# Kernel optimization log

Hardware: AMD Instinct MI355X
Metric: run time of the kernel (lower is better)

## Reference

```python
import jax, jax.numpy as jnp
import numpy as np

D_MODEL, D_K, D_V, N_HEADS = 1024, 64, 64, 16
B, S = 2, 2048
LN_EPS = 1e-5


def setup_inputs() -> dict:
    key = jax.random.key(0)
    ks = jax.random.split(key, 12)
    s = 1.0 / np.sqrt(D_MODEL)
    inp = {
        "Q": jax.random.normal(ks[0], (B, S, D_MODEL), jnp.float32),
        "K": jax.random.normal(ks[1], (B, S, D_MODEL), jnp.float32),
        "V": jax.random.normal(ks[2], (B, S, D_MODEL), jnp.float32),
        "attn_mask": jax.random.bernoulli(ks[3], 0.1, (B, S, S)),
        "Wq": jax.random.uniform(ks[4], (D_MODEL, D_K * N_HEADS), jnp.float32, -s, s),
        "bq": jnp.zeros((D_K * N_HEADS,), jnp.float32),
        "Wk": jax.random.uniform(ks[5], (D_MODEL, D_K * N_HEADS), jnp.float32, -s, s),
        "bk": jnp.zeros((D_K * N_HEADS,), jnp.float32),
        "Wv": jax.random.uniform(ks[6], (D_MODEL, D_V * N_HEADS), jnp.float32, -s, s),
        "bv": jnp.zeros((D_V * N_HEADS,), jnp.float32),
        "Wo": jax.random.uniform(ks[7], (N_HEADS * D_V, D_MODEL), jnp.float32, -s, s),
        "bo": jnp.zeros((D_MODEL,), jnp.float32),
        "gamma": jnp.ones((D_MODEL,), jnp.float32),
        "beta": jnp.zeros((D_MODEL,), jnp.float32),
    }
    return inp


def reference(Q, K, V, attn_mask, Wq, bq, Wk, bk, Wv, bv, Wo, bo, gamma, beta):
    b, s, _ = Q.shape
    # projections -> [B, S, H, d]
    q = (Q @ Wq + bq).reshape(b, s, N_HEADS, D_K)
    k = (K @ Wk + bk).reshape(b, -1, N_HEADS, D_K)
    v = (V @ Wv + bv).reshape(b, -1, N_HEADS, D_V)
    # scores [B, H, Sq, Sk]
    scores = jnp.einsum("bqhd,bkhd->bhqk", q, k) / np.sqrt(D_K).astype(np.float32)
    scores = jnp.where(attn_mask[:, None, :, :], jnp.float32(-1e9), scores)
    attn = jax.nn.softmax(scores, axis=-1)
    context = jnp.einsum("bhqk,bkhd->bqhd", attn, v).reshape(b, s, N_HEADS * D_V)
    out = context @ Wo + bo + Q  # residual
    mu = jnp.mean(out, axis=-1, keepdims=True)
    var = jnp.var(out, axis=-1, keepdims=True)
    return (out - mu) * jax.lax.rsqrt(var + LN_EPS) * gamma + beta
```

## Files before the change

kernel.cpp:

```cpp
#include <hip/hip_runtime.h>
#include <hip/hip_bf16.h>
#include <math.h>


#define D_MODEL 1024
#define NHEADS  16
#define DHEAD   64
#define BATCH   2
#define SEQ     2048
#define MROWS   (BATCH * SEQ)
#define SCLF    0.18033688f

typedef __attribute__((ext_vector_type(8)))  short bf16x8;
typedef __attribute__((ext_vector_type(4)))  float f32x4;
typedef __attribute__((ext_vector_type(16))) float f32x16;

__device__ inline unsigned short f2bf(float f) {
    unsigned int u = __builtin_bit_cast(unsigned int, f);
    unsigned int r = (u + 0x7FFFu + ((u >> 16) & 1u)) >> 16;
    return (unsigned short)r;
}

__device__ inline unsigned cvtpk_bf16(float lo, float hi2) {
    unsigned r;
    asm("v_cvt_pk_bf16_f32 %0, %1, %2" : "=v"(r) : "v"(lo), "v"(hi2));
    return r;
}

__device__ inline void gload16(const unsigned short* g, unsigned short* lbase, int lane) {
#if __has_builtin(__builtin_amdgcn_global_load_lds)
    __builtin_amdgcn_global_load_lds(
        (const __attribute__((address_space(1))) unsigned int*)g,
        (__attribute__((address_space(3))) unsigned int*)lbase, 16, 0, 0);
#else
    *(bf16x8*)(lbase + lane * 8) = *(const bf16x8*)g;
#endif
}

__global__ __launch_bounds__(256) void detect_mask_par(
    const unsigned int* __restrict__ m, int nwords, int* __restrict__ flags)
{
    const int i = blockIdx.x * 256 + threadIdx.x;
    int a = 0, b = 0;
    if (i < nwords) {
        const unsigned int w = m[i];
        a = (w != 0u && w != 1u);
        b = (w != 0u && w != 0x3F800000u);
    }
    const int wa = (int)__any(a);
    const int wb = (int)__any(b);
    if ((threadIdx.x & 63) == 0) {
        if (wa) atomicOr(&flags[0], 1);
        if (wb) atomicOr(&flags[1], 1);
    }
}

__global__ __launch_bounds__(256) void pack_mask_ballot(
    const void* __restrict__ mask, const int* __restrict__ flags,
    unsigned long long* __restrict__ mbits, int nwords)
{
    const int lane   = threadIdx.x & 63;
    const int wv     = blockIdx.x * 4 + (threadIdx.x >> 6);
    const int nwaves = gridDim.x * 4;
    const int mf = (flags[0] == 0) ? 0 : (flags[1] == 0) ? 1 : 2;
    for (int w = wv; w < nwords; w += nwaves) {
        bool bit;
        if (mf == 0)      bit = ((const unsigned int*)mask)[(size_t)w * 64 + lane] != 0u;
        else if (mf == 1) bit = ((const float*)mask)[(size_t)w * 64 + lane] != 0.f;
        else              bit = ((const unsigned char*)mask)[(size_t)w * 64 + lane] != 0;
        const unsigned long long b = __ballot(bit);
        if (lane == 0) mbits[w] = b;
    }
}

__global__ __launch_bounds__(256) void cvt_all(
    const float* __restrict__ Q, const float* __restrict__ K,
    const float* __restrict__ V,
    const float* __restrict__ w0, const float* __restrict__ w1,
    const float* __restrict__ w2, const float* __restrict__ w3,
    unsigned short* __restrict__ Qb, unsigned short* __restrict__ Kb,
    unsigned short* __restrict__ Vb,
    unsigned short* __restrict__ t0, unsigned short* __restrict__ t1,
    unsigned short* __restrict__ t2, unsigned short* __restrict__ t3)
{
    __shared__ float tile[64][65];
    const int z = blockIdx.z;
    if (z < 3) {
        const float* s = (z == 0) ? Q : (z == 1) ? K : V;
        unsigned short* d = (z == 0) ? Qb : (z == 1) ? Kb : Vb;
        const int i = blockIdx.x * 256 + threadIdx.x;
        float4 a = ((const float4*)s)[i * 2];
        float4 b = ((const float4*)s)[i * 2 + 1];
        unsigned u0 = cvtpk_bf16(a.x, a.y);
        unsigned u1 = cvtpk_bf16(a.z, a.w);
        unsigned u2 = cvtpk_bf16(b.x, b.y);
        unsigned u3 = cvtpk_bf16(b.z, b.w);
        ((int4*)d)[i] = make_int4((int)u0, (int)u1, (int)u2, (int)u3);
    } else {
        if (blockIdx.x >= 256) return;
        const int wz = z - 3;
        const float* W = (wz == 0) ? w0 : (wz == 1) ? w1 : (wz == 2) ? w2 : w3;
        unsigned short* T = (wz == 0) ? t0 : (wz == 1) ? t1 : (wz == 2) ? t2 : t3;
        const int n0 = (blockIdx.x & 15) * 64;
        const int k0 = (blockIdx.x >> 4) * 64;
        const int t  = threadIdx.x;
        const int r  = t >> 4;
        const int c4 = (t & 15) * 4;
        #pragma unroll
        for (int u = 0; u < 4; ++u) {
            float4 v = *(const float4*)(W + (size_t)(k0 + r + u * 16) * D_MODEL + n0 + c4);
            tile[r + u * 16][c4 + 0] = v.x;
            tile[r + u * 16][c4 + 1] = v.y;
            tile[r + u * 16][c4 + 2] = v.z;
            tile[r + u * 16][c4 + 3] = v.w;
        }
        __syncthreads();
        #pragma unroll
        for (int u = 0; u < 4; ++u) {
            const int nr = r + u * 16;
            ushort4 o;
            o.x = f2bf(tile[c4 + 0][nr]);
            o.y = f2bf(tile[c4 + 1][nr]);
            o.z = f2bf(tile[c4 + 2][nr]);
            o.w = f2bf(tile[c4 + 3][nr]);
            *(ushort4*)(T + (size_t)(n0 + nr) * D_MODEL + k0 + c4) = o;
        }
    }
}

#define BKQ 32
__global__ __launch_bounds__(256, 1) void gemm_qkv(
    const unsigned short* __restrict__ A0, const unsigned short* __restrict__ A1,
    const unsigned short* __restrict__ A2,
    const unsigned short* __restrict__ B0, const unsigned short* __restrict__ B1,
    const unsigned short* __restrict__ B2,
    const float* __restrict__ bias0, const float* __restrict__ bias1,
    const float* __restrict__ bias2,
    unsigned short* __restrict__ C0, unsigned short* __restrict__ C1,
    unsigned short* __restrict__ C2)
{
    const int z = blockIdx.z;
    const unsigned short* A  = (z == 0) ? A0 : (z == 1) ? A1 : A2;
    const unsigned short* Bt = (z == 0) ? B0 : (z == 1) ? B1 : B2;
    const float* bias        = (z == 0) ? bias0 : (z == 1) ? bias1 : bias2;
    unsigned short* C        = (z == 0) ? C0 : (z == 1) ? C1 : C2;
    const int K = D_MODEL, N = D_MODEL;

    __shared__ unsigned short As[2][128 * BKQ];
    __shared__ unsigned short Bs[2][128 * BKQ];
    const int tid  = threadIdx.x;
    const int w    = tid >> 6;
    const int lane = tid & 63;
    const int lo   = lane & 15;
    const int hi   = lane >> 4;
    const int wm   = (w >> 1) * 64;
    const int wn   = (w & 1) * 64;
    const int m0   = blockIdx.x * 128;
    const int n0   = blockIdx.y * 128;

    const unsigned short* Ab = A  + (size_t)m0 * K;
    const unsigned short* Bb = Bt + (size_t)n0 * K;

    f32x4 acc[4][4];
    #pragma unroll
    for (int i = 0; i < 4; ++i)
        #pragma unroll
        for (int j = 0; j < 4; ++j) acc[i][j] = (f32x4){0.f, 0.f, 0.f, 0.f};

    const int NT = K / BKQ;
    auto stage = [&](int buf, int t) {
        const int k0 = t * BKQ;
        #pragma unroll
        for (int i = 0; i < 2; ++i) {
            const int c = i * 256 + tid;
            gload16(Ab + (size_t)(c >> 2) * K + k0 + (c & 3) * 8,
                    &As[buf][(i * 256 + w * 64) * 8], lane);
        }
        #pragma unroll
        for (int i = 0; i < 2; ++i) {
            const int c = i * 256 + tid;
            gload16(Bb + (size_t)(c >> 2) * K + k0 + (c & 3) * 8,
                    &Bs[buf][(i * 256 + w * 64) * 8], lane);
        }
    };

    stage(0, 0);
    __syncthreads();
    int cur = 0;
    for (int t = 0; t < NT; ++t) {
        if (t + 1 < NT) stage(cur ^ 1, t + 1);
        bf16x8 af[4], bfr[4];
        #pragma unroll
        for (int f = 0; f < 4; ++f) {
            af[f]  = *(const bf16x8*)&As[cur][(wm + f * 16 + lo) * BKQ + hi * 8];
            bfr[f] = *(const bf16x8*)&Bs[cur][(wn + f * 16 + lo) * BKQ + hi * 8];
        }
        #pragma unroll
        for (int fm = 0; fm < 4; ++fm)
            #pragma unroll
            for (int fn = 0; fn < 4; ++fn)
                acc[fm][fn] = __builtin_amdgcn_mfma_f32_16x16x32_bf16(
                    af[fm], bfr[fn], acc[fm][fn], 0, 0, 0);
        __syncthreads();
        cur ^= 1;
    }

    #pragma unroll
    for (int fm = 0; fm < 4; ++fm) {
        const int row = m0 + wm + fm * 16 + hi * 4;
        #pragma unroll
        for (int fn = 0; fn < 4; ++fn) {
            const int col = n0 + wn + fn * 16 + lo;
            const float bv = bias[col];
            #pragma unroll
            for (int r = 0; r < 4; ++r) {
                float o = acc[fm][fn][r] + bv;
                if (z == 0) o *= SCLF;
                if (z < 2)
                    C[(size_t)(row + r) * N + col] = f2bf(o);
                else
                    C[(size_t)((row + r) >> 11) * 2097152
                      + (size_t)col * 2048 + ((row + r) & 2047)] = f2bf(o);
            }
        }
    }
}

__global__ __launch_bounds__(256) void gemm_out32(
    const unsigned short* __restrict__ A, const unsigned short* __restrict__ Bt,
    const float* __restrict__ bias, const float* __restrict__ resid,
    float* __restrict__ C)
{
    const int K = D_MODEL, N = D_MODEL;
    __shared__ unsigned short As[2][64 * 32];
    __shared__ unsigned short Bs[2][64 * 32];
    const int tid  = threadIdx.x;
    const int w    = tid >> 6;
    const int lane = tid & 63;
    const int lo   = lane & 15;
    const int hi   = lane >> 4;
    const int wm   = (w >> 1) * 32;
    const int wn   = (w & 1) * 32;
    const int m0   = blockIdx.x * 64;
    const int n0   = blockIdx.y * 64;

    const unsigned short* Ab = A  + (size_t)m0 * K;
    const unsigned short* Bb = Bt + (size_t)n0 * K;

    f32x4 acc[2][2];
    #pragma unroll
    for (int i = 0; i < 2; ++i)
        #pragma unroll
        for (int j = 0; j < 2; ++j) acc[i][j] = (f32x4){0.f, 0.f, 0.f, 0.f};

    const int NT = K / 32;
    auto stage = [&](int buf, int t) {
        const int k0 = t * 32;
        gload16(Ab + (size_t)(tid >> 2) * K + k0 + (tid & 3) * 8,
                &As[buf][(w * 64) * 8], lane);
        gload16(Bb + (size_t)(tid >> 2) * K + k0 + (tid & 3) * 8,
                &Bs[buf][(w * 64) * 8], lane);
    };

    stage(0, 0);
    __syncthreads();
    int cur = 0;
    for (int t = 0; t < NT; ++t) {
        if (t + 1 < NT) stage(cur ^ 1, t + 1);
        bf16x8 af[2], bfr[2];
        #pragma unroll
        for (int f = 0; f < 2; ++f) {
            af[f]  = *(const bf16x8*)&As[cur][(wm + f * 16 + lo) * 32 + hi * 8];
            bfr[f] = *(const bf16x8*)&Bs[cur][(wn + f * 16 + lo) * 32 + hi * 8];
        }
        #pragma unroll
        for (int fm = 0; fm < 2; ++fm)
            #pragma unroll
            for (int fn = 0; fn < 2; ++fn)
                acc[fm][fn] = __builtin_amdgcn_mfma_f32_16x16x32_bf16(
                    af[fm], bfr[fn], acc[fm][fn], 0, 0, 0);
        __syncthreads();
        cur ^= 1;
    }

    #pragma unroll
    for (int fm = 0; fm < 2; ++fm) {
        const int row = m0 + wm + fm * 16 + hi * 4;
        #pragma unroll
        for (int fn = 0; fn < 2; ++fn) {
            const int col = n0 + wn + fn * 16 + lo;
            const float bv = bias[col];
            #pragma unroll
            for (int r = 0; r < 4; ++r)
                C[(size_t)(row + r) * N + col] =
                    acc[fm][fn][r] + bv + resid[(size_t)(row + r) * N + col];
        }
    }
}

__global__ __launch_bounds__(512, 2) void attn_mfma32(
    const unsigned short* __restrict__ qb, const unsigned short* __restrict__ kbm,
    const unsigned short* __restrict__ vt,
    const unsigned long long* __restrict__ mbits, unsigned short* __restrict__ ctx)
{
    __shared__ __align__(16) unsigned char smem[34304];
    const int tid  = threadIdx.x;
    const int w8   = tid >> 6;
    const int g    = w8 >> 2;
    const int wq   = w8 & 3;
    const int lane = tid & 63;
    const int l31  = lane & 31;
    const int hi   = lane >> 5;
    const int h    = blockIdx.x;
    const int q0   = blockIdx.y * 128;
    const int b    = blockIdx.z;

    unsigned short* KsG = (unsigned short*)smem + (size_t)g * 4096;
    unsigned short* VsG = (unsigned short*)(smem + 16384) + (size_t)g * 4096;

    const size_t qkbase = (size_t)b * SEQ * D_MODEL + (size_t)h * DHEAD;
    const size_t vtbase = ((size_t)b * D_MODEL + h * DHEAD) * SEQ;

    const int qtok = q0 + wq * 32 + l31;
    bf16x8 qA[4];
    #pragma unroll
    for (int s = 0; s < 4; ++s)
        qA[s] = *(const bf16x8*)(qb + qkbase + (size_t)qtok * D_MODEL + s * 16 + hi * 8);

    const int4 ones_i = make_int4(0x3F803F80, 0x3F803F80, 0x3F803F80, 0x3F803F80);
    const bf16x8 ones = __builtin_bit_cast(bf16x8, ones_i);

    f32x16 o0 = {}, o1 = {}, accl = {};

    const unsigned long long* mrow = mbits + ((size_t)b * SEQ + qtok) * (SEQ / 64);

    const int krow = wq * 8 + (lane >> 3);
    const int kc   = lane & 7;
    const int kswz = kc ^ (krow & 7);
    const int vrow = wq * 16 + (lane >> 2);
    const int vsrc = ((lane & 3) - (vrow >> 1)) & 3;

    const unsigned short* kl = kbm + qkbase + (size_t)(g * 1024 + krow) * D_MODEL + kswz * 8;
    const unsigned short* vl = vt + vtbase + (size_t)vrow * SEQ + g * 1024 + vsrc * 8;
    const int kldb = (wq * 8) * 64;
    const int vldb = (wq * 16) * 32;

    auto stage = [&](int buf) {
        gload16(kl, &KsG[buf * 2048 + kldb], lane);
        gload16(vl, &VsG[buf * 2048 + vldb], lane);
        kl += (size_t)32 * D_MODEL;
        vl += 32;
    };

    stage(0);
    unsigned long long mw64 = mrow[g * 16];
    __syncthreads();
    int cur = 0;

    for (int t = 0; t < 32; ++t) {
        if (t + 1 < 32) stage(cur ^ 1);
        const unsigned int mw = (unsigned int)(mw64 >> (32 * (t & 1) + 4 * hi));
        if ((t & 1) && t + 1 < 32) mw64 = mrow[g * 16 + ((t + 1) >> 1)];

        f32x16 st = {};
        __builtin_amdgcn_s_setprio(1);
        #pragma unroll
        for (int s = 0; s < 4; ++s) {
            bf16x8 kf = *(const bf16x8*)&KsG[cur * 2048 + l31 * 64 + ((2 * s + hi) ^ (l31 & 7)) * 8];
            st = __builtin_amdgcn_mfma_f32_32x32x16_bf16(kf, qA[s], st, 0, 0, 0);
        }
        __builtin_amdgcn_s_setprio(0);

        #pragma unroll
        for (int r = 0; r < 16; ++r) {
            const int klo = (r & 3) + 8 * (r >> 2);
            const float x = ((mw >> klo) & 1u) ? -1e9f : st[r];
            st[r] = exp2f(x);
        }

        bf16x8 pa[2];
        #pragma unroll
        for (int s = 0; s < 2; ++s) {
            const int base = s * 8;
            unsigned av  = cvtpk_bf16(st[base + 0], st[base + 1]);
            unsigned bv2 = cvtpk_bf16(st[base + 4], st[base + 5]);
            unsigned cv  = cvtpk_bf16(st[base + 2], st[base + 3]);
            unsigned dv  = cvtpk_bf16(st[base + 6], st[base + 7]);
            asm("v_permlane32_swap_b32 %0, %1" : "+v"(av), "+v"(bv2));
            asm("v_permlane32_swap_b32 %0, %1" : "+v"(cv), "+v"(dv));
            int4 pk = make_int4((int)av, (int)cv, (int)bv2, (int)dv);
            pa[s] = __builtin_bit_cast(bf16x8, pk);
        }

        __builtin_amdgcn_s_setprio(1);
        #pragma unroll
        for (int s = 0; s < 2; ++s) {
            const int slot = ((2 * s + hi) + (l31 >> 1)) & 3;
            bf16x8 vf0 = *(const bf16x8*)&VsG[cur * 2048 + l31 * 32 + slot * 8];
            o0 = __builtin_amdgcn_mfma_f32_32x32x16_bf16(pa[s], vf0, o0, 0, 0, 0);
            bf16x8 vf1 = *(const bf16x8*)&VsG[cur * 2048 + (32 + l31) * 32 + slot * 8];
            o1 = __builtin_amdgcn_mfma_f32_32x32x16_bf16(pa[s], vf1, o1, 0, 0, 0);
            accl = __builtin_amdgcn_mfma_f32_32x32x16_bf16(pa[s], ones, accl, 0, 0, 0);
        }
        __builtin_amdgcn_s_setprio(0);
        __syncthreads();
        cur ^= 1;
    }

    __syncthreads();
    float* comb  = (float*)smem;
    float* lvals = (float*)(smem + 33792);
    if (g == 1) {
        float* p = comb + (size_t)(wq * 64 + lane) * 33;
        #pragma unroll
        for (int r = 0; r < 16; ++r) { p[r] = o0[r]; p[16 + r] = o1[r]; }
        if (l31 == 0) {
            #pragma unroll
            for (int r = 0; r < 16; ++r)
                lvals[wq * 32 + (r & 3) + 8 * (r >> 2) + 4 * hi] = accl[r];
        }
    }
    __syncthreads();
    if (g == 0) {
        const float* p = comb + (size_t)(wq * 64 + lane) * 33;
        #pragma unroll
        for (int r = 0; r < 16; ++r) {
            const int qloc = (r & 3) + 8 * (r >> 2) + 4 * hi;
            const float inv = 1.f / (accl[r] + lvals[wq * 32 + qloc]);
            unsigned short* dst = ctx + qkbase + (size_t)(q0 + wq * 32 + qloc) * D_MODEL;
            dst[l31]      = f2bf((o0[r] + p[r]) * inv);
            dst[32 + l31] = f2bf((o1[r] + p[16 + r]) * inv);
        }
    }
}

__global__ __launch_bounds__(256) void layernorm1024(
    const float* __restrict__ x, const float* __restrict__ gamma,
    const float* __restrict__ beta, float* __restrict__ out)
{
    const int row = blockIdx.x;
    const int tid = threadIdx.x;
    const float* xr = x + (size_t)row * D_MODEL;
    float4 v = *(const float4*)(xr + (tid << 2));
    float s = v.x + v.y + v.z + v.w;
    float q = v.x * v.x + v.y * v.y + v.z * v.z + v.w * v.w;
    #pragma unroll
    for (int off = 1; off < 64; off <<= 1) {
        s += __shfl_xor(s, off, 64);
        q += __shfl_xor(q, off, 64);
    }
    __shared__ float sw[4], qw_[4];
    const int wid = tid >> 6;
    if ((tid & 63) == 0) { sw[wid] = s; qw_[wid] = q; }
    __syncthreads();
    s = sw[0] + sw[1] + sw[2] + sw[3];
    q = qw_[0] + qw_[1] + qw_[2] + qw_[3];
    const float mu  = s * (1.f / D_MODEL);
    const float var = q * (1.f / D_MODEL) - mu * mu;
    const float a = var + 1e-5f;
    float inv = rsqrtf(a);
    inv = inv * (1.5f - 0.5f * a * inv * inv);
    float4 gg = *(const float4*)(gamma + (tid << 2));
    float4 bt = *(const float4*)(beta + (tid << 2));
    float4 o;
    o.x = (v.x - mu) * inv * gg.x + bt.x;
    o.y = (v.y - mu) * inv * gg.y + bt.y;
    o.z = (v.z - mu) * inv * gg.z + bt.z;
    o.w = (v.w - mu) * inv * gg.w + bt.w;
    *(float4*)(out + (size_t)row * D_MODEL + (tid << 2)) = o;
}

extern "C" void kernel_launch(void* const* d_in, const int* in_sizes, int n_in,
                              void* d_out, int out_size, void* d_ws, size_t ws_size,
                              hipStream_t stream)
{
    const float* Q    = (const float*)d_in[0];
    const float* K    = (const float*)d_in[1];
    const float* V    = (const float*)d_in[2];
    const void*  mask = d_in[3];
    const float* Wq   = (const float*)d_in[4];
    const float* bq   = (const float*)d_in[5];
    const float* Wk   = (const float*)d_in[6];
    const float* bk   = (const float*)d_in[7];
    const float* Wv   = (const float*)d_in[8];
    const float* bv   = (const float*)d_in[9];
    const float* Wo   = (const float*)d_in[10];
    const float* bo   = (const float*)d_in[11];
    const float* gam  = (const float*)d_in[12];
    const float* bet  = (const float*)d_in[13];
    float* out = (float*)d_out;

    const size_t NE = (size_t)MROWS * D_MODEL;
    const size_t WE = (size_t)D_MODEL * D_MODEL;
    const size_t NMW = (size_t)BATCH * SEQ * (SEQ / 64);
    unsigned short* Qbf = (unsigned short*)d_ws;
    unsigned short* Kbf = Qbf + NE;
    unsigned short* Vbf = Kbf + NE;
    unsigned short* qb  = Vbf + NE;
    unsigned short* kb  = qb + NE;
    unsigned short* vt  = kb + NE;
    unsigned short* Wt0 = vt + NE;
    unsigned short* Wt1 = Wt0 + WE;
    unsigned short* Wt2 = Wt1 + WE;
    unsigned short* Wt3 = Wt2 + WE;
    unsigned long long* mbits = (unsigned long long*)(Wt3 + WE);
    int* mflags = (int*)(mbits + NMW);
    unsigned short* ctxb = Qbf;
    float* outp = (float*)Kbf;
    if (ws_size < 6 * NE * 2 + 4 * WE * 2 + NMW * 8 + 64) return;

    hipMemsetAsync(mflags, 0, 2 * sizeof(int), stream);
    detect_mask_par<<<256, 256, 0, stream>>>((const unsigned int*)mask, 65536, mflags);
    pack_mask_ballot<<<2048, 256, 0, stream>>>(mask, mflags, mbits, (int)NMW);

    cvt_all<<<dim3(2048, 1, 7), 256, 0, stream>>>(Q, K, V, Wq, Wk, Wv, Wo,
                                                  Qbf, Kbf, Vbf, Wt0, Wt1, Wt2, Wt3);

    gemm_qkv<<<dim3(32, 8, 3), 256, 0, stream>>>(Qbf, Kbf, Vbf, Wt0, Wt1, Wt2,
                                                 bq, bk, bv, qb, kb, vt);

    dim3 ag(NHEADS, SEQ / 128, BATCH);
    attn_mfma32<<<ag, 512, 0, stream>>>(qb, kb, vt, mbits, ctxb);

    gemm_out32<<<dim3(64, 16), 256, 0, stream>>>(ctxb, Wt3, bo, Q, outp);

    layernorm1024<<<MROWS, 256, 0, stream>>>(outp, gam, bet, out);
}
```

Measured before the change: 180.9 us.

## Fuse mask packing into conversion kernel and shrink attention blocks to 64 queries

Moves the mask-packing ballot loop into the cvt_all kernel as an extra z-slice, removing one kernel launch. The attention kernel now uses 256 threads per block covering 64 query rows instead of 512 threads covering 128. Each wave stages two K/V rows so the shared K/V tiles still load fully. The aim is smaller blocks with higher occupancy and more blocks in the grid. The trade-off is that K/V tiles are loaded twice as often overall, since fewer queries share each loaded tile.

```diff
diff --git a/kernel.cpp b/kernel.cpp
--- a/kernel.cpp
+++ b/kernel.cpp
@@ -55,24 +55,6 @@
     }
 }
 
-__global__ __launch_bounds__(256) void pack_mask_ballot(
-    const void* __restrict__ mask, const int* __restrict__ flags,
-    unsigned long long* __restrict__ mbits, int nwords)
-{
-    const int lane   = threadIdx.x & 63;
-    const int wv     = blockIdx.x * 4 + (threadIdx.x >> 6);
-    const int nwaves = gridDim.x * 4;
-    const int mf = (flags[0] == 0) ? 0 : (flags[1] == 0) ? 1 : 2;
-    for (int w = wv; w < nwords; w += nwaves) {
-        bool bit;
-        if (mf == 0)      bit = ((const unsigned int*)mask)[(size_t)w * 64 + lane] != 0u;
-        else if (mf == 1) bit = ((const float*)mask)[(size_t)w * 64 + lane] != 0.f;
-        else              bit = ((const unsigned char*)mask)[(size_t)w * 64 + lane] != 0;
-        const unsigned long long b = __ballot(bit);
-        if (lane == 0) mbits[w] = b;
-    }
-}
-
 __global__ __launch_bounds__(256) void cvt_all(
     const float* __restrict__ Q, const float* __restrict__ K,
     const float* __restrict__ V,
@@ -81,7 +63,9 @@
     unsigned short* __restrict__ Qb, unsigned short* __restrict__ Kb,
     unsigned short* __restrict__ Vb,
     unsigned short* __restrict__ t0, unsigned short* __restrict__ t1,
-    unsigned short* __restrict__ t2, unsigned short* __restrict__ t3)
+    unsigned short* __restrict__ t2, unsigned short* __restrict__ t3,
+    const void* __restrict__ mask, const int* __restrict__ flags,
+    unsigned long long* __restrict__ mbits, int nwords)
 {
     __shared__ float tile[64][65];
     const int z = blockIdx.z;
@@ -96,7 +80,7 @@
         unsigned u2 = cvtpk_bf16(b.x, b.y);
         unsigned u3 = cvtpk_bf16(b.z, b.w);
         ((int4*)d)[i] = make_int4((int)u0, (int)u1, (int)u2, (int)u3);
-    } else {
+    } else if (z < 7) {
         if (blockIdx.x >= 256) return;
         const int wz = z - 3;
         const float* W = (wz == 0) ? w0 : (wz == 1) ? w1 : (wz == 2) ? w2 : w3;
@@ -124,6 +108,19 @@
             o.z = f2bf(tile[c4 + 2][nr]);
             o.w = f2bf(tile[c4 + 3][nr]);
             *(ushort4*)(T + (size_t)(n0 + nr) * D_MODEL + k0 + c4) = o;
+        }
+    } else {
+        const int lane   = threadIdx.x & 63;
+        const int wv     = blockIdx.x * 4 + (threadIdx.x >> 6);
+        const int nwaves = gridDim.x * 4;
+        const int mf = (flags[0] == 0) ? 0 : (flags[1] == 0) ? 1 : 2;
+        for (int w = wv; w < nwords; w += nwaves) {
+            bool bit;
+            if (mf == 0)      bit = ((const unsigned int*)mask)[(size_t)w * 64 + lane] != 0u;
+            else if (mf == 1) bit = ((const float*)mask)[(size_t)w * 64 + lane] != 0.f;
+            else              bit = ((const unsigned char*)mask)[(size_t)w * 64 + lane] != 0;
+            const unsigned long long bb = __ballot(bit);
+            if (lane == 0) mbits[w] = bb;
         }
     }
 }
@@ -298,21 +295,21 @@
     }
 }
 
-__global__ __launch_bounds__(512, 2) void attn_mfma32(
+__global__ __launch_bounds__(256, 4) void attn_mfma32(
     const unsigned short* __restrict__ qb, const unsigned short* __restrict__ kbm,
     const unsigned short* __restrict__ vt,
     const unsigned long long* __restrict__ mbits, unsigned short* __restrict__ ctx)
 {
-    __shared__ __align__(16) unsigned char smem[34304];
+    __shared__ __align__(16) unsigned char smem[32768];
     const int tid  = threadIdx.x;
-    const int w8   = tid >> 6;
-    const int g    = w8 >> 2;
-    const int wq   = w8 & 3;
+    const int w4   = tid >> 6;
+    const int g    = w4 >> 1;
+    const int wq   = w4 & 1;
     const int lane = tid & 63;
     const int l31  = lane & 31;
     const int hi   = lane >> 5;
     const int h    = blockIdx.x;
-    const int q0   = blockIdx.y * 128;
+    const int q0   = blockIdx.y * 64;
     const int b    = blockIdx.z;
 
     unsigned short* KsG = (unsigned short*)smem + (size_t)g * 4096;
@@ -334,22 +331,27 @@
 
     const unsigned long long* mrow = mbits + ((size_t)b * SEQ + qtok) * (SEQ / 64);
 
-    const int krow = wq * 8 + (lane >> 3);
-    const int kc   = lane & 7;
-    const int kswz = kc ^ (krow & 7);
-    const int vrow = wq * 16 + (lane >> 2);
-    const int vsrc = ((lane & 3) - (vrow >> 1)) & 3;
-
-    const unsigned short* kl = kbm + qkbase + (size_t)(g * 1024 + krow) * D_MODEL + kswz * 8;
-    const unsigned short* vl = vt + vtbase + (size_t)vrow * SEQ + g * 1024 + vsrc * 8;
-    const int kldb = (wq * 8) * 64;
-    const int vldb = (wq * 16) * 32;
+    const int krA = wq * 8 + (lane >> 3);
+    const int ksw = (lane & 7) ^ (krA & 7);
+    const int vrA = wq * 16 + (lane >> 2);
+    const int vsw = ((lane & 3) - (vrA >> 1)) & 3;
+
+    const unsigned short* klA = kbm + qkbase + (size_t)(g * 1024 + krA) * D_MODEL + ksw * 8;
+    const unsigned short* klB = klA + (size_t)16 * D_MODEL;
+    const unsigned short* vlA = vt + vtbase + (size_t)vrA * SEQ + g * 1024 + vsw * 8;
+    const unsigned short* vlB = vlA + (size_t)32 * SEQ;
+    const int kbA = (wq * 8) * 64, kbB = (16 + wq * 8) * 64;
+    const int vbA = (wq * 16) * 32, vbB = (32 + wq * 16) * 32;
 
     auto stage = [&](int buf) {
-        gload16(kl, &KsG[buf * 2048 + kldb], lane);
-        gload16(vl, &VsG[buf * 2048 + vldb], lane);
-        kl += (size_t)32 * D_MODEL;
-        vl += 32;
+        gload16(klA, &KsG[buf * 2048 + kbA], lane);
+        gload16(klB, &KsG[buf * 2048 + kbB], lane);
+        gload16(vlA, &VsG[buf * 2048 + vbA], lane);
+        gload16(vlB, &VsG[buf * 2048 + vbB], lane);
+        klA += (size_t)32 * D_MODEL;
+        klB += (size_t)32 * D_MODEL;
+        vlA += 32;
+        vlB += 32;
     };
 
     stage(0);
@@ -409,7 +411,7 @@
 
     __syncthreads();
     float* comb  = (float*)smem;
-    float* lvals = (float*)(smem + 33792);
+    float* lvals = (float*)(smem + 16896);
     if (g == 1) {
         float* p = comb + (size_t)(wq * 64 + lane) * 33;
         #pragma unroll
@@ -511,16 +513,16 @@
 
     hipMemsetAsync(mflags, 0, 2 * sizeof(int), stream);
     detect_mask_par<<<256, 256, 0, stream>>>((const unsigned int*)mask, 65536, mflags);
-    pack_mask_ballot<<<2048, 256, 0, stream>>>(mask, mflags, mbits, (int)NMW);
-
-    cvt_all<<<dim3(2048, 1, 7), 256, 0, stream>>>(Q, K, V, Wq, Wk, Wv, Wo,
-                                                  Qbf, Kbf, Vbf, Wt0, Wt1, Wt2, Wt3);
+
+    cvt_all<<<dim3(2048, 1, 8), 256, 0, stream>>>(Q, K, V, Wq, Wk, Wv, Wo,
+                                                  Qbf, Kbf, Vbf, Wt0, Wt1, Wt2, Wt3,
+                                                  mask, mflags, mbits, (int)NMW);
 
     gemm_qkv<<<dim3(32, 8, 3), 256, 0, stream>>>(Qbf, Kbf, Vbf, Wt0, Wt1, Wt2,
                                                  bq, bk, bv, qb, kb, vt);
 
-    dim3 ag(NHEADS, SEQ / 128, BATCH);
-    attn_mfma32<<<ag, 512, 0, stream>>>(qb, kb, vt, mbits, ctxb);
+    dim3 ag(NHEADS, SEQ / 64, BATCH);
+    attn_mfma32<<<ag, 256, 0, stream>>>(qb, kb, vt, mbits, ctxb);
 
     gemm_out32<<<dim3(64, 16), 256, 0, stream>>>(ctxb, Wt3, bo, Q, outp);
 
```

Result: slower. 186.7 us (+3.2%).
